# Kernel tuning notes

Measured on AMD Instinct MI355X. Metric: run time of the kernel, lower is better.

The kernel has to match this reference:

```python
import jax, jax.numpy as jnp
import numpy as np
import math

EMBED = 512
HEADS = 2
HEAD_DIM = EMBED // HEADS
EPS = 1e-5

def layer_norm(x, g, b):
    mu = jnp.mean(x, axis=-1, keepdims=True)
    var = jnp.var(x, axis=-1, keepdims=True)
    return (x - mu) * jax.lax.rsqrt(var + EPS) * g + b

def setup_inputs() -> dict:
    key = jax.random.key(0)
    ks = jax.random.split(key, 16)
    s = 0.02
    inp = {
        "text_embeds": jax.random.normal(ks[0], (128, 32, EMBED), jnp.float32),
        "video_embeds": jax.random.normal(ks[1], (64, 12, EMBED), jnp.float32),
        "ln1_g": jnp.ones((EMBED,), jnp.float32),
        "ln1_b": jnp.zeros((EMBED,), jnp.float32),
        "Wq": jax.random.normal(ks[2], (EMBED, EMBED), jnp.float32) * s,
        "bq": jnp.zeros((EMBED,), jnp.float32),
        "Wk": jax.random.normal(ks[3], (EMBED, EMBED), jnp.float32) * s,
        "bk": jnp.zeros((EMBED,), jnp.float32),
        "Wv": jax.random.normal(ks[4], (EMBED, EMBED), jnp.float32) * s,
        "bv": jnp.zeros((EMBED,), jnp.float32),
        "Wo": jax.random.normal(ks[5], (EMBED, EMBED), jnp.float32) * s,
        "bo": jnp.zeros((EMBED,), jnp.float32),
        "Wl": jax.random.normal(ks[6], (EMBED, EMBED), jnp.float32) * s,
        "bl": jnp.zeros((EMBED,), jnp.float32),
        "ln2_g": jnp.ones((EMBED,), jnp.float32),
        "ln2_b": jnp.zeros((EMBED,), jnp.float32),
        "ln3_g": jnp.ones((EMBED,), jnp.float32),
        "ln3_b": jnp.zeros((EMBED,), jnp.float32),
    }
    return inp

def reference(text_embeds, video_embeds, ln1_g, ln1_b, Wq, bq, Wk, bk, Wv, bv,
              Wo, bo, Wl, bl, ln2_g, ln2_b, ln3_g, ln3_b):
    # shared layer_norm1 on both modalities
    t = layer_norm(text_embeds, ln1_g, ln1_b)    # [T, Nw, E]
    vd = layer_norm(video_embeds, ln1_g, ln1_b)  # [V, F, E]
    T, Nw, _ = t.shape
    V, Fr, _ = vd.shape
    q = (t @ Wq.T + bq).reshape(T, Nw, HEADS, HEAD_DIM)   # bthd
    k = (vd @ Wk.T + bk).reshape(V, Fr, HEADS, HEAD_DIM)  # avhd
    v = (vd @ Wv.T + bv).reshape(V, Fr, HEADS, HEAD_DIM)  # avhd
    # cross-modal outer-product attention logits: [V, T, H, F, Nw]
    logits = jnp.einsum('avhd,bthd->abhvt', k, q) / math.sqrt(HEAD_DIM)
    weights = jax.nn.softmax(logits, axis=3)  # softmax over frames
    attn = jnp.einsum('avhd,abhvt->abhtd', v, weights)  # [V, T, H, Nw, D]
    attn = attn.transpose(0, 1, 3, 2, 4).reshape(V, T, Nw, EMBED)
    attn = attn.mean(axis=0)                    # [T, Nw, E]
    o = attn @ Wo.T + bo
    o = layer_norm(o, ln2_g, ln2_b)
    lin = o @ Wl.T + bl  # dropout is identity in eval mode
    out = layer_norm(o + lin, ln3_g, ln3_b)
    return out
```

## Files before the change

kernel.cpp:

```cpp
#include <hip/hip_runtime.h>
#include <math.h>

#define EMBED 512
#define HD 256
#define FR 12
#define NV 64
#define NT_TOK 4096
#define NV_TOK 768

#define WAIT_VM6 0x0F76
#define WAIT_VM0 0x0F70

typedef __attribute__((ext_vector_type(8))) short short8;
typedef __attribute__((ext_vector_type(4))) float f32x4;

__device__ __forceinline__ unsigned int f2bf(float f) {
  unsigned int u = __float_as_uint(f);
  u += 0x7FFFu + ((u >> 16) & 1u);
  return u >> 16;
}
__device__ __forceinline__ float bf2f(unsigned int h) {
  return __uint_as_float(h << 16);
}
__device__ __forceinline__ void async_cp16(void* lds, const void* g) {
  __builtin_amdgcn_global_load_lds(
      (const __attribute__((address_space(1))) void*)g,
      (__attribute__((address_space(3))) void*)lds, 16, 0, 0);
}

__device__ __forceinline__ void gemm_core(
    const unsigned short* __restrict__ Ab, int lda,
    const unsigned short* __restrict__ Bb, int ldb,
    int m0, int n0, int K,
    unsigned short* __restrict__ As, unsigned short* __restrict__ Bs,
    f32x4 acc[4][2]) {
  int tid = threadIdx.x;
  int w = tid >> 6, lane = tid & 63;
  int lr = lane & 15, quad = lane >> 4;
  int wm = (w >> 1) * 64, wn = (w & 1) * 32;
  int rowA[4], cgA[4], rowB[2], cgB[2];
  #pragma unroll
  for (int i = 0; i < 4; ++i) {
    int s = tid + i * 256;
    rowA[i] = s >> 3; cgA[i] = (s & 7) ^ (rowA[i] & 7);
  }
  #pragma unroll
  for (int i = 0; i < 2; ++i) {
    int s = tid + i * 256;
    rowB[i] = s >> 3; cgB[i] = (s & 7) ^ (rowB[i] & 7);
  }
  int nk = K >> 6;
  #pragma unroll
  for (int i = 0; i < 4; ++i)
    async_cp16(&As[(tid + i * 256) * 8],
               Ab + (size_t)(m0 + rowA[i]) * lda + cgA[i] * 8);
  #pragma unroll
  for (int i = 0; i < 2; ++i)
    async_cp16(&Bs[(tid + i * 256) * 8],
               Bb + (size_t)(n0 + rowB[i]) * ldb + cgB[i] * 8);
  for (int k = 0; k < nk; ++k) {
    int cur = k & 1;
    __builtin_amdgcn_s_barrier();
    if (k + 1 < nk) {
      int nxt = cur ^ 1;
      int koff = (k + 1) << 6;
      #pragma unroll
      for (int i = 0; i < 4; ++i)
        async_cp16(&As[nxt * 8192 + (tid + i * 256) * 8],
                   Ab + (size_t)(m0 + rowA[i]) * lda + koff + cgA[i] * 8);
      #pragma unroll
      for (int i = 0; i < 2; ++i)
        async_cp16(&Bs[nxt * 4096 + (tid + i * 256) * 8],
                   Bb + (size_t)(n0 + rowB[i]) * ldb + koff + cgB[i] * 8);
      __builtin_amdgcn_s_waitcnt(WAIT_VM6);
    } else {
      __builtin_amdgcn_s_waitcnt(WAIT_VM0);
    }
    __builtin_amdgcn_s_barrier();
    const unsigned short* Ac = As + cur * 8192;
    const unsigned short* Bc = Bs + cur * 4096;
    #pragma unroll
    for (int kk = 0; kk < 2; ++kk) {
      int sw = ((kk * 4 + quad) ^ (lr & 7)) * 8;
      short8 b0 = *(const short8*)&Bc[(wn + lr) * 64 + sw];
      short8 b1 = *(const short8*)&Bc[(wn + 16 + lr) * 64 + sw];
      #pragma unroll
      for (int i = 0; i < 4; ++i) {
        short8 a = *(const short8*)&Ac[(wm + i * 16 + lr) * 64 + sw];
        acc[i][0] = __builtin_amdgcn_mfma_f32_16x16x32_bf16(a, b0, acc[i][0], 0, 0, 0);
        acc[i][1] = __builtin_amdgcn_mfma_f32_16x16x32_bf16(a, b1, acc[i][1], 0, 0, 0);
      }
    }
  }
}

template <bool OUT_BF, bool BIAS>
__global__ __launch_bounds__(256) void gemm128(
    const unsigned short* __restrict__ A, int lda, long AzS,
    const unsigned short* __restrict__ B, int ldb, long BzS,
    const float* __restrict__ bias, void* __restrict__ Cv, int ldc, long CzS,
    int K) {
  __shared__ __align__(16) unsigned short As[2 * 128 * 64];
  __shared__ __align__(16) unsigned short Bs[2 * 64 * 64];
  f32x4 acc[4][2] = {};
  const unsigned short* Ab = A + (size_t)blockIdx.z * AzS;
  const unsigned short* Bb = B + (size_t)blockIdx.z * BzS;
  int m0 = blockIdx.x * 128, n0 = blockIdx.y * 64;
  gemm_core(Ab, lda, Bb, ldb, m0, n0, K, As, Bs, acc);
  int w = threadIdx.x >> 6, lane = threadIdx.x & 63;
  int lr = lane & 15, quad = lane >> 4;
  int wm = (w >> 1) * 64, wn = (w & 1) * 32;
  long cz = (long)blockIdx.z * CzS;
  #pragma unroll
  for (int j = 0; j < 2; ++j) {
    int col = n0 + wn + j * 16 + lr;
    float bv = BIAS ? bias[col] : 0.0f;
    #pragma unroll
    for (int i = 0; i < 4; ++i) {
      int rbase = m0 + wm + i * 16 + quad * 4;
      #pragma unroll
      for (int r = 0; r < 4; ++r) {
        float v = acc[i][j][r] + bv;
        if (OUT_BF)
          ((unsigned short*)Cv)[cz + (size_t)(rbase + r) * ldc + col] =
              (unsigned short)f2bf(v);
        else
          ((float*)Cv)[cz + (size_t)(rbase + r) * ldc + col] = v;
      }
    }
  }
}

__global__ __launch_bounds__(256) void qkv_kernel(
    const unsigned short* __restrict__ tn, const unsigned short* __restrict__ vn,
    const unsigned short* __restrict__ Wq, const unsigned short* __restrict__ Wk,
    const unsigned short* __restrict__ Wv,
    const float* __restrict__ bq, const float* __restrict__ bk,
    const float* __restrict__ bv,
    unsigned short* __restrict__ Q, unsigned short* __restrict__ Kout,
    unsigned short* __restrict__ Vt) {
  __shared__ __align__(16) unsigned short As[2 * 128 * 64];
  __shared__ __align__(16) unsigned short Bs[2 * 64 * 64];
  int bid = blockIdx.x;
  const unsigned short *Ap, *Bp;
  const float* bias;
  unsigned short* outp = nullptr;
  int m0, n0, mode;
  if (bid < 256) {
    Ap = tn; Bp = Wq; bias = bq; outp = Q;
    m0 = (bid >> 3) * 128; n0 = (bid & 7) * 64; mode = 0;
  } else if (bid < 304) {
    int i = bid - 256;
    Ap = vn; Bp = Wk; bias = bk; outp = Kout;
    m0 = (i >> 3) * 128; n0 = (i & 7) * 64; mode = 0;
  } else {
    int i = bid - 304;
    Ap = vn; Bp = Wv; bias = bv;
    m0 = (i >> 3) * 128; n0 = (i & 7) * 64; mode = 1;
  }
  f32x4 acc[4][2] = {};
  gemm_core(Ap, EMBED, Bp, EMBED, m0, n0, EMBED, As, Bs, acc);
  int w = threadIdx.x >> 6, lane = threadIdx.x & 63;
  int lr = lane & 15, quad = lane >> 4;
  int wm = (w >> 1) * 64, wn = (w & 1) * 32;
  #pragma unroll
  for (int j = 0; j < 2; ++j) {
    int col = n0 + wn + j * 16 + lr;
    float bvv = bias[col];
    #pragma unroll
    for (int i = 0; i < 4; ++i) {
      int rbase = m0 + wm + i * 16 + quad * 4;
      if (mode == 0) {
        #pragma unroll
        for (int r = 0; r < 4; ++r)
          outp[(size_t)(rbase + r) * EMBED + col] =
              (unsigned short)f2bf(acc[i][j][r] + bvv);
      } else {
        ushort4 pk;
        pk.x = (unsigned short)f2bf(acc[i][j][0] + bvv);
        pk.y = (unsigned short)f2bf(acc[i][j][1] + bvv);
        pk.z = (unsigned short)f2bf(acc[i][j][2] + bvv);
        pk.w = (unsigned short)f2bf(acc[i][j][3] + bvv);
        *(ushort4*)&Vt[(size_t)col * NV_TOK + rbase] = pk;
      }
    }
  }
}

__device__ __forceinline__ void ln_row(
    const float* __restrict__ xr, const float* __restrict__ rr,
    const float* __restrict__ g, const float* __restrict__ b,
    float* __restrict__ outf, unsigned short* __restrict__ outb) {
  int t = threadIdx.x;
  float v0 = xr[t], v1 = xr[t + 256];
  if (rr != nullptr) { v0 += rr[t]; v1 += rr[t + 256]; }
  float s = v0 + v1;
  float s2 = v0 * v0 + v1 * v1;
  #pragma unroll
  for (int off = 32; off > 0; off >>= 1) {
    s += __shfl_down(s, off, 64);
    s2 += __shfl_down(s2, off, 64);
  }
  __shared__ float ss[4], ss2[4];
  __shared__ float mean_s, rstd_s;
  int wid = t >> 6;
  if ((t & 63) == 0) { ss[wid] = s; ss2[wid] = s2; }
  __syncthreads();
  if (t == 0) {
    float a = ss[0] + ss[1] + ss[2] + ss[3];
    float a2 = ss2[0] + ss2[1] + ss2[2] + ss2[3];
    float mean = a * (1.0f / EMBED);
    float var = a2 * (1.0f / EMBED) - mean * mean;
    mean_s = mean;
    rstd_s = rsqrtf(var + 1e-5f);
  }
  __syncthreads();
  float mean = mean_s, rstd = rstd_s;
  float y0 = (v0 - mean) * rstd * g[t] + b[t];
  float y1 = (v1 - mean) * rstd * g[t + 256] + b[t + 256];
  if (outf != nullptr) { outf[t] = y0; outf[t + 256] = y1; }
  if (outb != nullptr) {
    outb[t] = (unsigned short)f2bf(y0);
    outb[t + 256] = (unsigned short)f2bf(y1);
  }
}

__global__ __launch_bounds__(256) void ln_kernel(
    const float* __restrict__ x, const float* __restrict__ res,
    const float* __restrict__ g, const float* __restrict__ b,
    float* __restrict__ outf, unsigned short* __restrict__ outb) {
  size_t row = blockIdx.x;
  ln_row(x + row * EMBED, res ? res + row * EMBED : nullptr, g, b,
         outf ? outf + row * EMBED : nullptr,
         outb ? outb + row * EMBED : nullptr);
}

__global__ __launch_bounds__(256) void prep_kernel(
    const float* __restrict__ text, const float* __restrict__ video,
    const float* __restrict__ g, const float* __restrict__ b,
    const float* __restrict__ Wq, const float* __restrict__ Wk,
    const float* __restrict__ Wv, const float* __restrict__ Wo,
    const float* __restrict__ Wl, unsigned short* __restrict__ Wbf,
    unsigned short* __restrict__ tn, unsigned short* __restrict__ vn) {
  int bid = blockIdx.x;
  if (bid < 1280) {
    int i = bid * 256 + threadIdx.x;
    const float* srcs[5] = {Wq, Wk, Wv, Wo, Wl};
    const float* src = srcs[i >> 16];
    float4 v = ((const float4*)src)[i & 65535];
    uint2 o;
    o.x = f2bf(v.x) | (f2bf(v.y) << 16);
    o.y = f2bf(v.z) | (f2bf(v.w) << 16);
    ((uint2*)Wbf)[i] = o;
    return;
  }
  if (bid < 1280 + NT_TOK) {
    size_t row = bid - 1280;
    ln_row(text + row * EMBED, nullptr, g, b, nullptr, tn + row * EMBED);
  } else {
    size_t row = bid - (1280 + NT_TOK);
    ln_row(video + row * EMBED, nullptr, g, b, nullptr, vn + row * EMBED);
  }
}

__global__ __launch_bounds__(256) void softmax12_kernel(unsigned short* __restrict__ S) {
  __shared__ uint2 buf[768];
  int t = threadIdx.x;
  uint2* g = (uint2*)S + (size_t)blockIdx.x * 768;
  #pragma unroll
  for (int i = 0; i < 3; ++i) buf[t + i * 256] = g[t + i * 256];
  __syncthreads();
  uint2 u0 = buf[t * 3], u1 = buf[t * 3 + 1], u2 = buf[t * 3 + 2];
  float v[12];
  v[0] = bf2f(u0.x & 0xffff); v[1] = bf2f(u0.x >> 16);
  v[2] = bf2f(u0.y & 0xffff); v[3] = bf2f(u0.y >> 16);
  v[4] = bf2f(u1.x & 0xffff); v[5] = bf2f(u1.x >> 16);
  v[6] = bf2f(u1.y & 0xffff); v[7] = bf2f(u1.y >> 16);
  v[8] = bf2f(u2.x & 0xffff); v[9] = bf2f(u2.x >> 16);
  v[10] = bf2f(u2.y & 0xffff); v[11] = bf2f(u2.y >> 16);
  float m = -1e30f;
  #pragma unroll
  for (int f = 0; f < FR; ++f) { v[f] *= 0.0625f; m = fmaxf(m, v[f]); }
  float s = 0.f;
  #pragma unroll
  for (int f = 0; f < FR; ++f) { v[f] = __expf(v[f] - m); s += v[f]; }
  float inv = (1.0f / NV) / s;
  unsigned int w[12];
  #pragma unroll
  for (int f = 0; f < FR; ++f) w[f] = f2bf(v[f] * inv);
  uint2 o0, o1, o2;
  o0.x = w[0] | (w[1] << 16);  o0.y = w[2] | (w[3] << 16);
  o1.x = w[4] | (w[5] << 16);  o1.y = w[6] | (w[7] << 16);
  o2.x = w[8] | (w[9] << 16);  o2.y = w[10] | (w[11] << 16);
  buf[t * 3] = o0; buf[t * 3 + 1] = o1; buf[t * 3 + 2] = o2;
  __syncthreads();
  #pragma unroll
  for (int i = 0; i < 3; ++i) g[t + i * 256] = buf[t + i * 256];
}

extern "C" void kernel_launch(void* const* d_in, const int* in_sizes, int n_in,
                              void* d_out, int out_size, void* d_ws, size_t ws_size,
                              hipStream_t stream) {
  (void)in_sizes; (void)n_in; (void)out_size; (void)ws_size;
  const float* text  = (const float*)d_in[0];
  const float* video = (const float*)d_in[1];
  const float* ln1_g = (const float*)d_in[2];
  const float* ln1_b = (const float*)d_in[3];
  const float* Wq = (const float*)d_in[4];
  const float* bq = (const float*)d_in[5];
  const float* Wk = (const float*)d_in[6];
  const float* bk = (const float*)d_in[7];
  const float* Wv = (const float*)d_in[8];
  const float* bv = (const float*)d_in[9];
  const float* Wo = (const float*)d_in[10];
  const float* bo = (const float*)d_in[11];
  const float* Wl = (const float*)d_in[12];
  const float* bl = (const float*)d_in[13];
  const float* ln2_g = (const float*)d_in[14];
  const float* ln2_b = (const float*)d_in[15];
  const float* ln3_g = (const float*)d_in[16];
  const float* ln3_b = (const float*)d_in[17];
  float* out = (float*)d_out;

  char* base = (char*)d_ws;
  unsigned short* Wbf   = (unsigned short*)base;
  unsigned short* Wq_bf = Wbf + 0 * 262144;
  unsigned short* Wk_bf = Wbf + 1 * 262144;
  unsigned short* Wv_bf = Wbf + 2 * 262144;
  unsigned short* Wo_bf = Wbf + 3 * 262144;
  unsigned short* Wl_bf = Wbf + 4 * 262144;
  unsigned short* Vt    = (unsigned short*)(base + 2621440);
  char* big = base + 3407872;
  unsigned short* Q_bf   = (unsigned short*)(big + 0);
  unsigned short* K_bf   = (unsigned short*)(big + 4194304);
  unsigned short* S      = (unsigned short*)(big + 4980736);
  unsigned short* tn_bf  = (unsigned short*)(big + 17563648);
  unsigned short* vn_bf  = (unsigned short*)(big + 21757952);
  unsigned short* att_bf = (unsigned short*)(big + 17563648);
  float*          Ob     = (float*)(big + 4980736);
  float*          o2f    = (float*)(big + 13369344);
  unsigned short* o2_bf  = (unsigned short*)(big + 21757952);
  float*          lin    = (float*)(big + 0);

  prep_kernel<<<1280 + NT_TOK + NV_TOK, 256, 0, stream>>>(
      text, video, ln1_g, ln1_b, Wq, Wk, Wv, Wo, Wl, Wbf, tn_bf, vn_bf);

  qkv_kernel<<<352, 256, 0, stream>>>(tn_bf, vn_bf, Wq_bf, Wk_bf, Wv_bf,
                                      bq, bk, bv, Q_bf, K_bf, Vt);

  gemm128<true, false><<<dim3(32, 12, 2), 256, 0, stream>>>(
      Q_bf, EMBED, HD, K_bf, EMBED, HD, nullptr, S, NV_TOK,
      (long)NT_TOK * NV_TOK, HD);
  softmax12_kernel<<<2048, 256, 0, stream>>>(S);
  gemm128<true, false><<<dim3(32, 4, 2), 256, 0, stream>>>(
      S, NV_TOK, (long)NT_TOK * NV_TOK, Vt, NV_TOK, (long)HD * NV_TOK, nullptr,
      att_bf, EMBED, HD, NV_TOK);

  gemm128<false, true><<<dim3(32, 8, 1), 256, 0, stream>>>(
      att_bf, EMBED, 0, Wo_bf, EMBED, 0, bo, Ob, EMBED, 0, EMBED);
  ln_kernel<<<NT_TOK, 256, 0, stream>>>(Ob, nullptr, ln2_g, ln2_b, o2f, o2_bf);
  gemm128<false, true><<<dim3(32, 8, 1), 256, 0, stream>>>(
      o2_bf, EMBED, 0, Wl_bf, EMBED, 0, bl, lin, EMBED, 0, EMBED);
  ln_kernel<<<NT_TOK, 256, 0, stream>>>(o2f, lin, ln3_g, ln3_b, out, nullptr);
}
```

Measured before the change: 171.4 us.

## Fuse QK^T logits GEMM with frame softmax and shrink GEMM tiles to 64x64

Adds a sgemm_softmax kernel that computes a 64x96 logits tile per block, stages it in LDS, and applies the 12-frame softmax with the 1/NV mean scale before writing bf16 weights. This removes the separate softmax kernel and its full read-modify-write pass over the large logits buffer. All other GEMMs, including the fused QKV kernel, move from 128x64 to 64x64 tiles with launch_bounds(256,4) for more blocks and higher occupancy. The explicit vmcnt waits are replaced by __syncthreads, which may serialise the async copy pipeline more conservatively, and smaller tiles reduce reuse per block.

```diff
diff --git a/kernel.cpp b/kernel.cpp
--- a/kernel.cpp
+++ b/kernel.cpp
@@ -8,9 +8,6 @@
 #define NT_TOK 4096
 #define NV_TOK 768
 
-#define WAIT_VM6 0x0F76
-#define WAIT_VM0 0x0F70
-
 typedef __attribute__((ext_vector_type(8))) short short8;
 typedef __attribute__((ext_vector_type(4))) float f32x4;
 
@@ -19,109 +16,94 @@
   u += 0x7FFFu + ((u >> 16) & 1u);
   return u >> 16;
 }
-__device__ __forceinline__ float bf2f(unsigned int h) {
-  return __uint_as_float(h << 16);
-}
 __device__ __forceinline__ void async_cp16(void* lds, const void* g) {
   __builtin_amdgcn_global_load_lds(
       (const __attribute__((address_space(1))) void*)g,
       (__attribute__((address_space(3))) void*)lds, 16, 0, 0);
 }
 
-__device__ __forceinline__ void gemm_core(
+__device__ __forceinline__ void gemm64_core(
     const unsigned short* __restrict__ Ab, int lda,
     const unsigned short* __restrict__ Bb, int ldb,
     int m0, int n0, int K,
     unsigned short* __restrict__ As, unsigned short* __restrict__ Bs,
-    f32x4 acc[4][2]) {
+    f32x4 acc[2][2]) {
   int tid = threadIdx.x;
   int w = tid >> 6, lane = tid & 63;
   int lr = lane & 15, quad = lane >> 4;
-  int wm = (w >> 1) * 64, wn = (w & 1) * 32;
-  int rowA[4], cgA[4], rowB[2], cgB[2];
-  #pragma unroll
-  for (int i = 0; i < 4; ++i) {
-    int s = tid + i * 256;
-    rowA[i] = s >> 3; cgA[i] = (s & 7) ^ (rowA[i] & 7);
-  }
+  int wm = (w >> 1) * 32, wn = (w & 1) * 32;
+  int rowS[2], cgS[2];
   #pragma unroll
   for (int i = 0; i < 2; ++i) {
     int s = tid + i * 256;
-    rowB[i] = s >> 3; cgB[i] = (s & 7) ^ (rowB[i] & 7);
+    rowS[i] = s >> 3; cgS[i] = (s & 7) ^ (rowS[i] & 7);
   }
   int nk = K >> 6;
   #pragma unroll
-  for (int i = 0; i < 4; ++i)
+  for (int i = 0; i < 2; ++i) {
     async_cp16(&As[(tid + i * 256) * 8],
-               Ab + (size_t)(m0 + rowA[i]) * lda + cgA[i] * 8);
-  #pragma unroll
-  for (int i = 0; i < 2; ++i)
+               Ab + (size_t)(m0 + rowS[i]) * lda + cgS[i] * 8);
     async_cp16(&Bs[(tid + i * 256) * 8],
-               Bb + (size_t)(n0 + rowB[i]) * ldb + cgB[i] * 8);
+               Bb + (size_t)(n0 + rowS[i]) * ldb + cgS[i] * 8);
+  }
   for (int k = 0; k < nk; ++k) {
     int cur = k & 1;
-    __builtin_amdgcn_s_barrier();
+    __syncthreads();
     if (k + 1 < nk) {
-      int nxt = cur ^ 1;
-      int koff = (k + 1) << 6;
+      int nxt = cur ^ 1, koff = (k + 1) << 6;
       #pragma unroll
-      for (int i = 0; i < 4; ++i)
-        async_cp16(&As[nxt * 8192 + (tid + i * 256) * 8],
-                   Ab + (size_t)(m0 + rowA[i]) * lda + koff + cgA[i] * 8);
-      #pragma unroll
-      for (int i = 0; i < 2; ++i)
+      for (int i = 0; i < 2; ++i) {
+        async_cp16(&As[nxt * 4096 + (tid + i * 256) * 8],
+                   Ab + (size_t)(m0 + rowS[i]) * lda + koff + cgS[i] * 8);
         async_cp16(&Bs[nxt * 4096 + (tid + i * 256) * 8],
-                   Bb + (size_t)(n0 + rowB[i]) * ldb + koff + cgB[i] * 8);
-      __builtin_amdgcn_s_waitcnt(WAIT_VM6);
-    } else {
-      __builtin_amdgcn_s_waitcnt(WAIT_VM0);
-    }
-    __builtin_amdgcn_s_barrier();
-    const unsigned short* Ac = As + cur * 8192;
+                   Bb + (size_t)(n0 + rowS[i]) * ldb + koff + cgS[i] * 8);
+      }
+    }
+    const unsigned short* Ac = As + cur * 4096;
     const unsigned short* Bc = Bs + cur * 4096;
     #pragma unroll
     for (int kk = 0; kk < 2; ++kk) {
       int sw = ((kk * 4 + quad) ^ (lr & 7)) * 8;
+      short8 a0 = *(const short8*)&Ac[(wm + lr) * 64 + sw];
+      short8 a1 = *(const short8*)&Ac[(wm + 16 + lr) * 64 + sw];
       short8 b0 = *(const short8*)&Bc[(wn + lr) * 64 + sw];
       short8 b1 = *(const short8*)&Bc[(wn + 16 + lr) * 64 + sw];
-      #pragma unroll
-      for (int i = 0; i < 4; ++i) {
-        short8 a = *(const short8*)&Ac[(wm + i * 16 + lr) * 64 + sw];
-        acc[i][0] = __builtin_amdgcn_mfma_f32_16x16x32_bf16(a, b0, acc[i][0], 0, 0, 0);
-        acc[i][1] = __builtin_amdgcn_mfma_f32_16x16x32_bf16(a, b1, acc[i][1], 0, 0, 0);
-      }
-    }
-  }
-}
-
-template <bool OUT_BF, bool BIAS>
-__global__ __launch_bounds__(256) void gemm128(
+      acc[0][0] = __builtin_amdgcn_mfma_f32_16x16x32_bf16(a0, b0, acc[0][0], 0, 0, 0);
+      acc[0][1] = __builtin_amdgcn_mfma_f32_16x16x32_bf16(a0, b1, acc[0][1], 0, 0, 0);
+      acc[1][0] = __builtin_amdgcn_mfma_f32_16x16x32_bf16(a1, b0, acc[1][0], 0, 0, 0);
+      acc[1][1] = __builtin_amdgcn_mfma_f32_16x16x32_bf16(a1, b1, acc[1][1], 0, 0, 0);
+    }
+  }
+}
+
+template <int MODE, bool BIAS>
+__global__ __launch_bounds__(256, 4) void gemm64(
     const unsigned short* __restrict__ A, int lda, long AzS,
     const unsigned short* __restrict__ B, int ldb, long BzS,
     const float* __restrict__ bias, void* __restrict__ Cv, int ldc, long CzS,
     int K) {
-  __shared__ __align__(16) unsigned short As[2 * 128 * 64];
-  __shared__ __align__(16) unsigned short Bs[2 * 64 * 64];
-  f32x4 acc[4][2] = {};
+  __shared__ __align__(16) unsigned short As[2 * 4096];
+  __shared__ __align__(16) unsigned short Bs[2 * 4096];
+  f32x4 acc[2][2] = {};
   const unsigned short* Ab = A + (size_t)blockIdx.z * AzS;
   const unsigned short* Bb = B + (size_t)blockIdx.z * BzS;
-  int m0 = blockIdx.x * 128, n0 = blockIdx.y * 64;
-  gemm_core(Ab, lda, Bb, ldb, m0, n0, K, As, Bs, acc);
+  int m0 = blockIdx.x * 64, n0 = blockIdx.y * 64;
+  gemm64_core(Ab, lda, Bb, ldb, m0, n0, K, As, Bs, acc);
   int w = threadIdx.x >> 6, lane = threadIdx.x & 63;
   int lr = lane & 15, quad = lane >> 4;
-  int wm = (w >> 1) * 64, wn = (w & 1) * 32;
+  int wm = (w >> 1) * 32, wn = (w & 1) * 32;
   long cz = (long)blockIdx.z * CzS;
   #pragma unroll
   for (int j = 0; j < 2; ++j) {
     int col = n0 + wn + j * 16 + lr;
     float bv = BIAS ? bias[col] : 0.0f;
     #pragma unroll
-    for (int i = 0; i < 4; ++i) {
+    for (int i = 0; i < 2; ++i) {
       int rbase = m0 + wm + i * 16 + quad * 4;
       #pragma unroll
       for (int r = 0; r < 4; ++r) {
         float v = acc[i][j][r] + bv;
-        if (OUT_BF)
+        if (MODE == 0)
           ((unsigned short*)Cv)[cz + (size_t)(rbase + r) * ldc + col] =
               (unsigned short)f2bf(v);
         else
@@ -131,7 +113,7 @@
   }
 }
 
-__global__ __launch_bounds__(256) void qkv_kernel(
+__global__ __launch_bounds__(256, 4) void qkv_kernel(
     const unsigned short* __restrict__ tn, const unsigned short* __restrict__ vn,
     const unsigned short* __restrict__ Wq, const unsigned short* __restrict__ Wk,
     const unsigned short* __restrict__ Wv,
@@ -139,36 +121,36 @@
     const float* __restrict__ bv,
     unsigned short* __restrict__ Q, unsigned short* __restrict__ Kout,
     unsigned short* __restrict__ Vt) {
-  __shared__ __align__(16) unsigned short As[2 * 128 * 64];
-  __shared__ __align__(16) unsigned short Bs[2 * 64 * 64];
+  __shared__ __align__(16) unsigned short As[2 * 4096];
+  __shared__ __align__(16) unsigned short Bs[2 * 4096];
   int bid = blockIdx.x;
   const unsigned short *Ap, *Bp;
   const float* bias;
   unsigned short* outp = nullptr;
   int m0, n0, mode;
-  if (bid < 256) {
+  if (bid < 512) {
     Ap = tn; Bp = Wq; bias = bq; outp = Q;
-    m0 = (bid >> 3) * 128; n0 = (bid & 7) * 64; mode = 0;
-  } else if (bid < 304) {
-    int i = bid - 256;
+    m0 = (bid >> 3) * 64; n0 = (bid & 7) * 64; mode = 0;
+  } else if (bid < 608) {
+    int i = bid - 512;
     Ap = vn; Bp = Wk; bias = bk; outp = Kout;
-    m0 = (i >> 3) * 128; n0 = (i & 7) * 64; mode = 0;
+    m0 = (i >> 3) * 64; n0 = (i & 7) * 64; mode = 0;
   } else {
-    int i = bid - 304;
+    int i = bid - 608;
     Ap = vn; Bp = Wv; bias = bv;
-    m0 = (i >> 3) * 128; n0 = (i & 7) * 64; mode = 1;
-  }
-  f32x4 acc[4][2] = {};
-  gemm_core(Ap, EMBED, Bp, EMBED, m0, n0, EMBED, As, Bs, acc);
+    m0 = (i >> 3) * 64; n0 = (i & 7) * 64; mode = 1;
+  }
+  f32x4 acc[2][2] = {};
+  gemm64_core(Ap, EMBED, Bp, EMBED, m0, n0, EMBED, As, Bs, acc);
   int w = threadIdx.x >> 6, lane = threadIdx.x & 63;
   int lr = lane & 15, quad = lane >> 4;
-  int wm = (w >> 1) * 64, wn = (w & 1) * 32;
+  int wm = (w >> 1) * 32, wn = (w & 1) * 32;
   #pragma unroll
   for (int j = 0; j < 2; ++j) {
     int col = n0 + wn + j * 16 + lr;
     float bvv = bias[col];
     #pragma unroll
-    for (int i = 0; i < 4; ++i) {
+    for (int i = 0; i < 2; ++i) {
       int rbase = m0 + wm + i * 16 + quad * 4;
       if (mode == 0) {
         #pragma unroll
@@ -183,6 +165,109 @@
         pk.w = (unsigned short)f2bf(acc[i][j][3] + bvv);
         *(ushort4*)&Vt[(size_t)col * NV_TOK + rbase] = pk;
       }
+    }
+  }
+}
+
+__global__ __launch_bounds__(256, 4) void sgemm_softmax(
+    const unsigned short* __restrict__ Q, const unsigned short* __restrict__ Kb,
+    unsigned short* __restrict__ P) {
+  __shared__ __align__(16) char smem[40960];
+  unsigned short* As = (unsigned short*)smem;
+  unsigned short* Bs = (unsigned short*)(smem + 16384);
+  int tid = threadIdx.x;
+  int w = tid >> 6, lane = tid & 63;
+  int lr = lane & 15, quad = lane >> 4;
+  int wm = (w >> 1) * 32, wn = (w & 1) * 48;
+  int h = blockIdx.z;
+  int m0 = blockIdx.x * 64, n0 = blockIdx.y * 96;
+  const unsigned short* Ab = Q + h * HD;
+  const unsigned short* Bb = Kb + h * HD;
+  int rowA[2], cgA[2], rowB[3], cgB[3];
+  #pragma unroll
+  for (int i = 0; i < 2; ++i) {
+    int s = tid + i * 256;
+    rowA[i] = s >> 3; cgA[i] = (s & 7) ^ (rowA[i] & 7);
+  }
+  #pragma unroll
+  for (int i = 0; i < 3; ++i) {
+    int s = tid + i * 256;
+    rowB[i] = s >> 3; cgB[i] = (s & 7) ^ (rowB[i] & 7);
+  }
+  f32x4 acc[2][3] = {};
+  const int nk = HD >> 6;
+  #pragma unroll
+  for (int i = 0; i < 2; ++i)
+    async_cp16(&As[(tid + i * 256) * 8],
+               Ab + (size_t)(m0 + rowA[i]) * EMBED + cgA[i] * 8);
+  #pragma unroll
+  for (int i = 0; i < 3; ++i)
+    async_cp16(&Bs[(tid + i * 256) * 8],
+               Bb + (size_t)(n0 + rowB[i]) * EMBED + cgB[i] * 8);
+  for (int k = 0; k < nk; ++k) {
+    int cur = k & 1;
+    __syncthreads();
+    if (k + 1 < nk) {
+      int nxt = cur ^ 1, koff = (k + 1) << 6;
+      #pragma unroll
+      for (int i = 0; i < 2; ++i)
+        async_cp16(&As[nxt * 4096 + (tid + i * 256) * 8],
+                   Ab + (size_t)(m0 + rowA[i]) * EMBED + koff + cgA[i] * 8);
+      #pragma unroll
+      for (int i = 0; i < 3; ++i)
+        async_cp16(&Bs[nxt * 6144 + (tid + i * 256) * 8],
+                   Bb + (size_t)(n0 + rowB[i]) * EMBED + koff + cgB[i] * 8);
+    }
+    const unsigned short* Ac = As + cur * 4096;
+    const unsigned short* Bc = Bs + cur * 6144;
+    #pragma unroll
+    for (int kk = 0; kk < 2; ++kk) {
+      int sw = ((kk * 4 + quad) ^ (lr & 7)) * 8;
+      short8 a0 = *(const short8*)&Ac[(wm + lr) * 64 + sw];
+      short8 a1 = *(const short8*)&Ac[(wm + 16 + lr) * 64 + sw];
+      short8 b0 = *(const short8*)&Bc[(wn + lr) * 64 + sw];
+      short8 b1 = *(const short8*)&Bc[(wn + 16 + lr) * 64 + sw];
+      short8 b2 = *(const short8*)&Bc[(wn + 32 + lr) * 64 + sw];
+      acc[0][0] = __builtin_amdgcn_mfma_f32_16x16x32_bf16(a0, b0, acc[0][0], 0, 0, 0);
+      acc[0][1] = __builtin_amdgcn_mfma_f32_16x16x32_bf16(a0, b1, acc[0][1], 0, 0, 0);
+      acc[0][2] = __builtin_amdgcn_mfma_f32_16x16x32_bf16(a0, b2, acc[0][2], 0, 0, 0);
+      acc[1][0] = __builtin_amdgcn_mfma_f32_16x16x32_bf16(a1, b0, acc[1][0], 0, 0, 0);
+      acc[1][1] = __builtin_amdgcn_mfma_f32_16x16x32_bf16(a1, b1, acc[1][1], 0, 0, 0);
+      acc[1][2] = __builtin_amdgcn_mfma_f32_16x16x32_bf16(a1, b2, acc[1][2], 0, 0, 0);
+    }
+  }
+  __syncthreads();
+  float* Sx = (float*)smem;
+  #pragma unroll
+  for (int j = 0; j < 3; ++j) {
+    int col = wn + j * 16 + lr;
+    #pragma unroll
+    for (int i = 0; i < 2; ++i) {
+      int rbase = wm + i * 16 + quad * 4;
+      #pragma unroll
+      for (int r = 0; r < 4; ++r) Sx[(rbase + r) * 100 + col] = acc[i][j][r];
+    }
+  }
+  __syncthreads();
+  unsigned short* Ph = P + (size_t)h * NT_TOK * NV_TOK;
+  #pragma unroll
+  for (int gi = 0; gi < 2; ++gi) {
+    int g = tid * 2 + gi;
+    int row = g >> 3, gr = g & 7;
+    const float* sp = Sx + row * 100 + gr * 12;
+    float v[12];
+    float m = -1e30f;
+    #pragma unroll
+    for (int f = 0; f < FR; ++f) { v[f] = sp[f] * 0.0625f; m = fmaxf(m, v[f]); }
+    float s = 0.f;
+    #pragma unroll
+    for (int f = 0; f < FR; ++f) { v[f] = __expf(v[f] - m); s += v[f]; }
+    float inv = (1.0f / NV) / s;
+    unsigned short* pp = Ph + (size_t)(m0 + row) * NV_TOK + n0 + gr * 12;
+    #pragma unroll
+    for (int ii = 0; ii < 6; ++ii) {
+      unsigned int lo = f2bf(v[2 * ii] * inv), hi = f2bf(v[2 * ii + 1] * inv);
+      *(unsigned int*)(pp + 2 * ii) = lo | (hi << 16);
     }
   }
 }
@@ -261,41 +346,6 @@
     size_t row = bid - (1280 + NT_TOK);
     ln_row(video + row * EMBED, nullptr, g, b, nullptr, vn + row * EMBED);
   }
-}
-
-__global__ __launch_bounds__(256) void softmax12_kernel(unsigned short* __restrict__ S) {
-  __shared__ uint2 buf[768];
-  int t = threadIdx.x;
-  uint2* g = (uint2*)S + (size_t)blockIdx.x * 768;
-  #pragma unroll
-  for (int i = 0; i < 3; ++i) buf[t + i * 256] = g[t + i * 256];
-  __syncthreads();
-  uint2 u0 = buf[t * 3], u1 = buf[t * 3 + 1], u2 = buf[t * 3 + 2];
-  float v[12];
-  v[0] = bf2f(u0.x & 0xffff); v[1] = bf2f(u0.x >> 16);
-  v[2] = bf2f(u0.y & 0xffff); v[3] = bf2f(u0.y >> 16);
-  v[4] = bf2f(u1.x & 0xffff); v[5] = bf2f(u1.x >> 16);
-  v[6] = bf2f(u1.y & 0xffff); v[7] = bf2f(u1.y >> 16);
-  v[8] = bf2f(u2.x & 0xffff); v[9] = bf2f(u2.x >> 16);
-  v[10] = bf2f(u2.y & 0xffff); v[11] = bf2f(u2.y >> 16);
-  float m = -1e30f;
-  #pragma unroll
-  for (int f = 0; f < FR; ++f) { v[f] *= 0.0625f; m = fmaxf(m, v[f]); }
-  float s = 0.f;
-  #pragma unroll
-  for (int f = 0; f < FR; ++f) { v[f] = __expf(v[f] - m); s += v[f]; }
-  float inv = (1.0f / NV) / s;
-  unsigned int w[12];
-  #pragma unroll
-  for (int f = 0; f < FR; ++f) w[f] = f2bf(v[f] * inv);
-  uint2 o0, o1, o2;
-  o0.x = w[0] | (w[1] << 16);  o0.y = w[2] | (w[3] << 16);
-  o1.x = w[4] | (w[5] << 16);  o1.y = w[6] | (w[7] << 16);
-  o2.x = w[8] | (w[9] << 16);  o2.y = w[10] | (w[11] << 16);
-  buf[t * 3] = o0; buf[t * 3 + 1] = o1; buf[t * 3 + 2] = o2;
-  __syncthreads();
-  #pragma unroll
-  for (int i = 0; i < 3; ++i) g[t + i * 256] = buf[t + i * 256];
 }
 
 extern "C" void kernel_launch(void* const* d_in, const int* in_sizes, int n_in,
@@ -331,35 +381,33 @@
   unsigned short* Wl_bf = Wbf + 4 * 262144;
   unsigned short* Vt    = (unsigned short*)(base + 2621440);
   char* big = base + 3407872;
-  unsigned short* Q_bf   = (unsigned short*)(big + 0);
-  unsigned short* K_bf   = (unsigned short*)(big + 4194304);
-  unsigned short* S      = (unsigned short*)(big + 4980736);
-  unsigned short* tn_bf  = (unsigned short*)(big + 17563648);
-  unsigned short* vn_bf  = (unsigned short*)(big + 21757952);
-  unsigned short* att_bf = (unsigned short*)(big + 17563648);
-  float*          Ob     = (float*)(big + 4980736);
-  float*          o2f    = (float*)(big + 13369344);
-  unsigned short* o2_bf  = (unsigned short*)(big + 21757952);
-  float*          lin    = (float*)(big + 0);
+  unsigned short* Q_bf  = (unsigned short*)(big + 0);
+  unsigned short* K_bf  = (unsigned short*)(big + 4194304);
+  unsigned short* P     = (unsigned short*)(big + 4980736);
+  unsigned short* tn_bf = (unsigned short*)(big + 17563648);
+  unsigned short* vn_bf = (unsigned short*)(big + 21757952);
+  unsigned short* att_bf = tn_bf;
+  float* Ob  = (float*)(big + 4980736);
+  float* o2f = (float*)(big + 13369344);
+  unsigned short* o2_bf = vn_bf;
+  float* lin = (float*)(big + 0);
 
   prep_kernel<<<1280 + NT_TOK + NV_TOK, 256, 0, stream>>>(
       text, video, ln1_g, ln1_b, Wq, Wk, Wv, Wo, Wl, Wbf, tn_bf, vn_bf);
 
-  qkv_kernel<<<352, 256, 0, stream>>>(tn_bf, vn_bf, Wq_bf, Wk_bf, Wv_bf,
+  qkv_kernel<<<704, 256, 0, stream>>>(tn_bf, vn_bf, Wq_bf, Wk_bf, Wv_bf,
                                       bq, bk, bv, Q_bf, K_bf, Vt);
 
-  gemm128<true, false><<<dim3(32, 12, 2), 256, 0, stream>>>(
-      Q_bf, EMBED, HD, K_bf, EMBED, HD, nullptr, S, NV_TOK,
-      (long)NT_TOK * NV_TOK, HD);
-  softmax12_kernel<<<2048, 256, 0, stream>>>(S);
-  gemm128<true, false><<<dim3(32, 4, 2), 256, 0, stream>>>(
-      S, NV_TOK, (long)NT_TOK * NV_TOK, Vt, NV_TOK, (long)HD * NV_TOK, nullptr,
+  sgemm_softmax<<<dim3(64, 8, 2), 256, 0, stream>>>(Q_bf, K_bf, P);
+
+  gemm64<0, false><<<dim3(64, 4, 2), 256, 0, stream>>>(
+      P, NV_TOK, (long)NT_TOK * NV_TOK, Vt, NV_TOK, (long)HD * NV_TOK, nullptr,
       att_bf, EMBED, HD, NV_TOK);
 
-  gemm128<false, true><<<dim3(32, 8, 1), 256, 0, stream>>>(
+  gemm64<1, true><<<dim3(64, 8, 1), 256, 0, stream>>>(
       att_bf, EMBED, 0, Wo_bf, EMBED, 0, bo, Ob, EMBED, 0, EMBED);
   ln_kernel<<<NT_TOK, 256, 0, stream>>>(Ob, nullptr, ln2_g, ln2_b, o2f, o2_bf);
-  gemm128<false, true><<<dim3(32, 8, 1), 256, 0, stream>>>(
+  gemm64<1, true><<<dim3(64, 8, 1), 256, 0, stream>>>(
       o2_bf, EMBED, 0, Wl_bf, EMBED, 0, bl, lin, EMBED, 0, EMBED);
   ln_kernel<<<NT_TOK, 256, 0, stream>>>(o2f, lin, ln3_g, ln3_b, out, nullptr);
 }
```

After: 162.7 us. 5.0% less time.
